# Optimization experiments

Measured on AMD Instinct MI355X. Metric: run time of the kernel, lower is better.

Reference implementation:

```python
import jax, jax.numpy as jnp
import numpy as np

NUM_HEADS = 4
WS = 3


def setup_inputs() -> dict:
    key = jax.random.key(0)
    k1, k2, k3 = jax.random.split(key, 3)
    B, Hs, Ws_, C = 16, 96, 96, 256
    x = jax.random.normal(k1, (B, Hs * Ws_, C), dtype=jnp.float32)
    # torch nn.Linear weights: [out_features, in_features]
    Wqkv = jax.random.normal(k2, (3 * C, C), dtype=jnp.float32) * (1.0 / np.sqrt(C))
    Wproj = jax.random.normal(k3, (C, C), dtype=jnp.float32) * (1.0 / np.sqrt(C))
    return {"x": x, "Wqkv": Wqkv, "Wproj": Wproj, "H": Hs, "W": Ws_}


def reference(x, Wqkv, Wproj, H, W):
    B, N, C = x.shape
    ws = WS
    nh = NUM_HEADS
    hd = C // nh
    scale = hd ** -0.5

    pad_h = (ws - H % ws) % ws
    pad_w = (ws - W % ws) % ws
    xg = x.reshape(B, H, W, C)
    if pad_h > 0 or pad_w > 0:
        xg = jnp.pad(xg, ((0, 0), (0, pad_h), (0, pad_w), (0, 0)))
    H_pad, W_pad = H + pad_h, W + pad_w
    nWh, nWw = H_pad // ws, W_pad // ws
    Bw = B * nWh * nWw

    # window partition: [B, nWh, ws, nWw, ws, C] -> [Bw, ws*ws, C]
    xw = xg.reshape(B, nWh, ws, nWw, ws, C).transpose(0, 1, 3, 2, 4, 5)
    xw = xw.reshape(Bw, ws * ws, C)

    # qkv projection (Linear, no bias): x @ W^T
    qkv = xw @ Wqkv.T                                   # [Bw, 9, 3C]
    qkv = qkv.reshape(Bw, ws * ws, 3, nh, hd).transpose(2, 0, 3, 1, 4)
    q, k, v = qkv[0], qkv[1], qkv[2]                    # [Bw, nh, 9, hd]

    attn = jnp.einsum("bhqd,bhkd->bhqk", q, k) * scale  # [Bw, nh, 9, 9]
    attn = jax.nn.softmax(attn, axis=-1)
    out = jnp.einsum("bhqk,bhkd->bhqd", attn, v)        # [Bw, nh, 9, hd]
    out = out.transpose(0, 2, 1, 3).reshape(Bw, ws * ws, C)
    out = out @ Wproj.T

    # window unpartition
    out = out.reshape(B, nWh, nWw, ws, ws, C).transpose(0, 1, 3, 2, 4, 5)
    out = out.reshape(B, H_pad, W_pad, C)
    if pad_h > 0 or pad_w > 0:
        out = out[:, :H, :W, :]
    return out.reshape(B, H * W, C)
```

## Files before the change

### kernel.cpp

```cpp
#include <hip/hip_runtime.h>
#include <hip/hip_bf16.h>

using f32x4  = __attribute__((ext_vector_type(4))) float;
using bf16x8 = __attribute__((ext_vector_type(8))) short;
using bf16x4 = __attribute__((ext_vector_type(4))) short;
using u32x2  = __attribute__((ext_vector_type(2))) unsigned int;
using u32x4  = __attribute__((ext_vector_type(4))) unsigned int;

__device__ __forceinline__ float bf2f(short s) {
    unsigned u = ((unsigned)(unsigned short)s) << 16;
    return __builtin_bit_cast(float, u);
}
__device__ __forceinline__ unsigned short f2b(float f) {
    unsigned u = __builtin_bit_cast(unsigned, f);
    unsigned r = u + 0x7FFFu + ((u >> 16) & 1u);
    return (unsigned short)(r >> 16);
}
__device__ __forceinline__ void gl_lds16(const void* g, void* l) {
    __builtin_amdgcn_global_load_lds((const __attribute__((address_space(1))) void*)g,
                                     (__attribute__((address_space(3))) void*)l, 16, 0, 0);
}

__global__ void k_wconv(const float* __restrict__ wq, const float* __restrict__ wp,
                        unsigned short* __restrict__ out) {
    int i = blockIdx.x * 256 + threadIdx.x;
    float v = (i < 196608) ? wq[i] : wp[i - 196608];
    out[i] = f2b(v);
}

__global__ __launch_bounds__(256, 3) void k_qkv3(
    const float* __restrict__ x,
    const unsigned short* __restrict__ wqkv,
    unsigned short* __restrict__ qkv)
{
    __shared__ unsigned short As[128 * 64];
    __shared__ unsigned short Bs[128 * 64];
    const int tid = threadIdx.x;
    const int wv = tid >> 6, ln = tid & 63;
    const int lr = ln & 15, lk = ln >> 4;
    const int l8 = ln >> 3, c8 = ln & 7;

    const int b = blockIdx.x;
    const int w = (b & 7) * 864 + (b >> 3);
    const size_t m0 = (size_t)(w / 6) * 128;
    const int n0 = (w % 6) * 128;
    const int mq = (wv >> 1) * 64, nq = (wv & 1) * 64;

    f32x4 acc[4][4];
#pragma unroll
    for (int mi = 0; mi < 4; ++mi)
#pragma unroll
        for (int ni = 0; ni < 4; ++ni) {
            f32x4 z = {0.f, 0.f, 0.f, 0.f};
            acc[mi][ni] = z;
        }

#pragma unroll 1
    for (int ks = 0; ks < 4; ++ks) {
        const int k0 = ks * 64;
        __syncthreads();
#pragma unroll
        for (int i = 0; i < 4; ++i) {
            int r8 = i * 8 + l8;
            int sc = (c8 ^ (r8 & 7)) * 8;
            gl_lds16(wqkv + (size_t)(n0 + wv * 32 + r8) * 256 + k0 + sc,
                     &Bs[(wv * 32 + i * 8) * 64]);
        }
#pragma unroll
        for (int i = 0; i < 4; ++i) {
            int slot = tid + 256 * i;
            int row = slot >> 3, ch = slot & 7;
            const f32x4* p = (const f32x4*)(x + (m0 + row) * 256 + k0 + ch * 8);
            f32x4 f0 = p[0], f1 = p[1];
            bf16x8 v;
#pragma unroll
            for (int j = 0; j < 4; ++j) {
                v[j]     = (short)f2b(f0[j]);
                v[4 + j] = (short)f2b(f1[j]);
            }
            *(bf16x8*)&As[row * 64 + ((ch ^ (row & 7)) * 8)] = v;
        }
        __syncthreads();

#pragma unroll
        for (int kk = 0; kk < 2; ++kk) {
            bf16x8 av[4], bv[4];
#pragma unroll
            for (int i = 0; i < 4; ++i) {
                int ar = mq + i * 16 + lr;
                av[i] = *(const bf16x8*)&As[ar * 64 + (((kk * 4 + lk) ^ (ar & 7)) * 8)];
                int br = nq + i * 16 + lr;
                bv[i] = *(const bf16x8*)&Bs[br * 64 + (((kk * 4 + lk) ^ (br & 7)) * 8)];
            }
#pragma unroll
            for (int mi = 0; mi < 4; ++mi)
#pragma unroll
                for (int ni = 0; ni < 4; ++ni)
                    acc[mi][ni] = __builtin_amdgcn_mfma_f32_16x16x32_bf16(bv[ni], av[mi], acc[mi][ni], 0, 0, 0);
        }
    }

#pragma unroll
    for (int mi = 0; mi < 4; ++mi) {
        const size_t row = m0 + mq + mi * 16 + lr;
#pragma unroll
        for (int ni = 0; ni < 4; ++ni) {
            u32x2 u;
            u[0] = (unsigned)f2b(acc[mi][ni][0]) | ((unsigned)f2b(acc[mi][ni][1]) << 16);
            u[1] = (unsigned)f2b(acc[mi][ni][2]) | ((unsigned)f2b(acc[mi][ni][3]) << 16);
            *(u32x2*)(qkv + row * 768 + n0 + nq + ni * 16 + lk * 4) = u;
        }
    }
}

__global__ __launch_bounds__(256) void k_attn(
    unsigned short* __restrict__ qkv)
{
    constexpr int LQ = 68;
    __shared__ unsigned short Ks[144 * LQ];
    __shared__ unsigned short Vs[144 * LQ];
    const int tid = threadIdx.x;
    const int t3 = blockIdx.x;
    const int hf = blockIdx.y;
    const int h  = blockIdx.z;
    const int bb = t3 >> 5, wh = t3 & 31;

    for (int idx = tid; idx < 1152; idx += 256) {
        int row = idx >> 3, ch = idx & 7;
        int ww = row / 9, t = row - ww * 9;
        int rr = t / 3, cc = t - rr * 3;
        size_t xrow = (size_t)bb * 9216 + (wh * 3 + rr) * 96 + hf * 48 + ww * 3 + cc;
        *(bf16x8*)&Ks[row * LQ + ch * 8] = *(const bf16x8*)(qkv + xrow * 768 + 256 + h * 64 + ch * 8);
        *(bf16x8*)&Vs[row * LQ + ch * 8] = *(const bf16x8*)(qkv + xrow * 768 + 512 + h * 64 + ch * 8);
    }
    __syncthreads();

#pragma unroll 1
    for (int pass = 0; pass < 2; ++pass) {
        int row;
        bool act;
        if (pass == 0) { row = tid >> 1;            act = true; }
        else           { row = 128 + (tid >> 1);    act = tid < 32; }
        if (act) {
            const int hc = tid & 1;
            const int w9 = (row / 9) * 9;
            int t = row - w9;
            int rr = t / 3, cc = t - rr * 3;
            size_t xrow = (size_t)bb * 9216 + (wh * 3 + rr) * 96 + hf * 48 + (w9 / 9) * 3 + cc;
            unsigned short* qp = qkv + xrow * 768 + h * 64 + hc * 32;
            float q[32];
#pragma unroll
            for (int g = 0; g < 4; ++g) {
                bf16x8 v = *(const bf16x8*)(qp + g * 8);
#pragma unroll
                for (int j = 0; j < 8; ++j) q[g * 8 + j] = bf2f(v[j]);
            }
            float s[9];
#pragma unroll
            for (int kk = 0; kk < 9; ++kk) {
                float acc = 0.f;
#pragma unroll
                for (int g = 0; g < 4; ++g) {
                    bf16x8 v = *(const bf16x8*)&Ks[(w9 + kk) * LQ + hc * 32 + g * 8];
#pragma unroll
                    for (int j = 0; j < 8; ++j) acc += q[g * 8 + j] * bf2f(v[j]);
                }
                s[kk] = acc;
            }
#pragma unroll
            for (int kk = 0; kk < 9; ++kk)
                s[kk] = (s[kk] + __shfl_xor(s[kk], 1)) * 0.125f;
            float m = s[0];
#pragma unroll
            for (int kk = 1; kk < 9; ++kk) m = fmaxf(m, s[kk]);
            float sum = 0.f;
#pragma unroll
            for (int kk = 0; kk < 9; ++kk) { s[kk] = __expf(s[kk] - m); sum += s[kk]; }
            float inv = 1.f / sum;
            float o[32];
#pragma unroll
            for (int d = 0; d < 32; ++d) o[d] = 0.f;
#pragma unroll
            for (int kk = 0; kk < 9; ++kk) {
                float pk = s[kk] * inv;
#pragma unroll
                for (int g = 0; g < 4; ++g) {
                    bf16x8 v = *(const bf16x8*)&Vs[(w9 + kk) * LQ + hc * 32 + g * 8];
#pragma unroll
                    for (int j = 0; j < 8; ++j) o[g * 8 + j] += pk * bf2f(v[j]);
                }
            }
#pragma unroll
            for (int grp = 0; grp < 4; ++grp) {
                u32x4 u;
#pragma unroll
                for (int e = 0; e < 4; ++e) {
                    int i0 = grp * 8 + e * 2;
                    u[e] = (unsigned)f2b(o[i0]) | ((unsigned)f2b(o[i0 + 1]) << 16);
                }
                *(u32x4*)(qp + grp * 8) = u;
            }
        }
    }
}

__global__ __launch_bounds__(256) void k_proj(
    const unsigned short* __restrict__ ain,
    const unsigned short* __restrict__ wproj,
    float* __restrict__ out)
{
    __shared__ unsigned short As[128 * 64];
    __shared__ unsigned short Bs[128 * 64];
    const int tid = threadIdx.x;
    const int wv = tid >> 6, ln = tid & 63;
    const int lr = ln & 15, lk = ln >> 4;
    const int l8 = ln >> 3, c8 = ln & 7;

    int b = blockIdx.x;
    int w = (b & 7) * 288 + (b >> 3);
    const size_t m0 = (size_t)(w >> 1) * 128;
    const int n0 = (w & 1) * 128;
    const int mq = (wv >> 1) * 64, nq = (wv & 1) * 64;

    f32x4 acc[4][4];
#pragma unroll
    for (int mi = 0; mi < 4; ++mi)
#pragma unroll
        for (int ni = 0; ni < 4; ++ni) {
            f32x4 z = {0.f, 0.f, 0.f, 0.f};
            acc[mi][ni] = z;
        }

#pragma unroll 1
    for (int ks = 0; ks < 4; ++ks) {
        const int k0 = ks * 64;
        __syncthreads();
#pragma unroll
        for (int i = 0; i < 4; ++i) {
            int r8 = i * 8 + l8;
            int sc = (c8 ^ (r8 & 7)) * 8;
            gl_lds16(ain   + (m0 + wv * 32 + r8) * 768 + k0 + sc,
                     &As[(wv * 32 + i * 8) * 64]);
            gl_lds16(wproj + (size_t)(n0 + wv * 32 + r8) * 256 + k0 + sc,
                     &Bs[(wv * 32 + i * 8) * 64]);
        }
        __syncthreads();

#pragma unroll
        for (int kk = 0; kk < 2; ++kk) {
            bf16x8 av[4], bv[4];
#pragma unroll
            for (int i = 0; i < 4; ++i) {
                int ar = mq + i * 16 + lr;
                av[i] = *(const bf16x8*)&As[ar * 64 + (((kk * 4 + lk) ^ (ar & 7)) * 8)];
                int br = nq + i * 16 + lr;
                bv[i] = *(const bf16x8*)&Bs[br * 64 + (((kk * 4 + lk) ^ (br & 7)) * 8)];
            }
#pragma unroll
            for (int mi = 0; mi < 4; ++mi)
#pragma unroll
                for (int ni = 0; ni < 4; ++ni)
                    acc[mi][ni] = __builtin_amdgcn_mfma_f32_16x16x32_bf16(bv[ni], av[mi], acc[mi][ni], 0, 0, 0);
        }
    }

#pragma unroll
    for (int mi = 0; mi < 4; ++mi) {
        const size_t row = m0 + mq + mi * 16 + lr;
#pragma unroll
        for (int ni = 0; ni < 4; ++ni)
            *(f32x4*)&out[row * 256 + n0 + nq + ni * 16 + lk * 4] = acc[mi][ni];
    }
}


__device__ __forceinline__ int grow_of(int wbase, int row) {
    int wi = row / 9;
    int t  = row - wi * 9;
    int w  = wbase + wi;
    if (w >= 16384) return -1;
    int b = w >> 10, rem = w & 1023;
    int wh = rem >> 5, ww = rem & 31;
    int r = t / 3, c = t - r * 3;
    return b * 9216 + (wh * 3 + r) * 96 + ww * 3 + c;
}

__global__ __launch_bounds__(256) void k_winattn_fb(
    const float* __restrict__ x,
    const unsigned short* __restrict__ wqkv,
    unsigned short* __restrict__ aout)
{
    constexpr int LDA = 264;
    constexpr int LQ  = 68;
    __shared__ unsigned short As[64 * LDA];
    __shared__ unsigned short Qb[3][64 * LQ];
    __shared__ int rowmap[64];

    const int tid = threadIdx.x;
    const int wbase = blockIdx.x * 7;
    const int wv = tid >> 6, ln = tid & 63;
    const int lr = ln & 15, lk = ln >> 4;
    const int mw = wv >> 1, nw = wv & 1;

    if (tid < 64)
        rowmap[tid] = (tid < 63) ? grow_of(wbase, tid) : -1;
    __syncthreads();

    for (int idx = tid; idx < 64 * 32; idx += 256) {
        int row = idx >> 5, g = idx & 31;
        int gr = rowmap[row];
        bf16x8 v;
        if (gr >= 0) {
            const f32x4* p = (const f32x4*)(x + (size_t)gr * 256 + g * 8);
            f32x4 f0 = p[0], f1 = p[1];
#pragma unroll
            for (int j = 0; j < 4; ++j) {
                v[j]     = (short)f2b(f0[j]);
                v[4 + j] = (short)f2b(f1[j]);
            }
        } else {
#pragma unroll
            for (int j = 0; j < 8; ++j) v[j] = 0;
        }
        *(bf16x8*)&As[row * LDA + g * 8] = v;
    }
    __syncthreads();

#pragma unroll 1
    for (int h = 0; h < 4; ++h) {
#pragma unroll 1
        for (int part = 0; part < 3; ++part) {
            const int j0 = part * 256 + h * 64 + nw * 32;
            bf16x8 w[2][8];
#pragma unroll
            for (int ni = 0; ni < 2; ++ni)
#pragma unroll
                for (int kk = 0; kk < 8; ++kk)
                    w[ni][kk] = *(const bf16x8*)(wqkv + (size_t)(j0 + ni * 16 + lr) * 256 + kk * 32 + lk * 8);

            f32x4 acc[2][2];
#pragma unroll
            for (int mi = 0; mi < 2; ++mi)
#pragma unroll
                for (int ni = 0; ni < 2; ++ni) {
                    f32x4 z = {0.f, 0.f, 0.f, 0.f};
                    acc[mi][ni] = z;
                }
#pragma unroll
            for (int kk = 0; kk < 8; ++kk) {
                const int k0 = kk * 32 + lk * 8;
                bf16x8 a0 = *(const bf16x8*)&As[(mw * 32 + lr) * LDA + k0];
                bf16x8 a1 = *(const bf16x8*)&As[(mw * 32 + 16 + lr) * LDA + k0];
                acc[0][0] = __builtin_amdgcn_mfma_f32_16x16x32_bf16(w[0][kk], a0, acc[0][0], 0, 0, 0);
                acc[1][0] = __builtin_amdgcn_mfma_f32_16x16x32_bf16(w[0][kk], a1, acc[1][0], 0, 0, 0);
                acc[0][1] = __builtin_amdgcn_mfma_f32_16x16x32_bf16(w[1][kk], a0, acc[0][1], 0, 0, 0);
                acc[1][1] = __builtin_amdgcn_mfma_f32_16x16x32_bf16(w[1][kk], a1, acc[1][1], 0, 0, 0);
            }
#pragma unroll
            for (int mi = 0; mi < 2; ++mi)
#pragma unroll
                for (int ni = 0; ni < 2; ++ni) {
                    int row = mw * 32 + mi * 16 + lr;
                    int col = nw * 32 + ni * 16 + lk * 4;
                    u32x2 u;
                    u[0] = (unsigned)f2b(acc[mi][ni][0]) | ((unsigned)f2b(acc[mi][ni][1]) << 16);
                    u[1] = (unsigned)f2b(acc[mi][ni][2]) | ((unsigned)f2b(acc[mi][ni][3]) << 16);
                    *(u32x2*)&Qb[part][row * LQ + col] = u;
                }
        }
        __syncthreads();
        {
            const int row = wv * 16 + lr;
            const int c   = lk;
            if (row < 63) {
                const int w9 = (row / 9) * 9;
                float q[16];
#pragma unroll
                for (int g = 0; g < 4; ++g) {
                    bf16x4 v = *(const bf16x4*)&Qb[0][row * LQ + c * 16 + g * 4];
#pragma unroll
                    for (int j = 0; j < 4; ++j) q[g * 4 + j] = bf2f(v[j]);
                }
                float s[9];
#pragma unroll
                for (int kk = 0; kk < 9; ++kk) {
                    float t = 0.f;
#pragma unroll
                    for (int g = 0; g < 4; ++g) {
                        bf16x4 v = *(const bf16x4*)&Qb[1][(w9 + kk) * LQ + c * 16 + g * 4];
#pragma unroll
                        for (int j = 0; j < 4; ++j) t += q[g * 4 + j] * bf2f(v[j]);
                    }
                    s[kk] = t;
                }
#pragma unroll
                for (int kk = 0; kk < 9; ++kk) {
                    float t = s[kk];
                    t += __shfl_xor(t, 16);
                    t += __shfl_xor(t, 32);
                    s[kk] = t * 0.125f;
                }
                float m = s[0];
#pragma unroll
                for (int kk = 1; kk < 9; ++kk) m = fmaxf(m, s[kk]);
                float sum = 0.f;
#pragma unroll
                for (int kk = 0; kk < 9; ++kk) { s[kk] = __expf(s[kk] - m); sum += s[kk]; }
                float inv = 1.f / sum;
                float o[16];
#pragma unroll
                for (int d = 0; d < 16; ++d) o[d] = 0.f;
#pragma unroll
                for (int kk = 0; kk < 9; ++kk) {
                    float pk = s[kk] * inv;
#pragma unroll
                    for (int g = 0; g < 4; ++g) {
                        bf16x4 v = *(const bf16x4*)&Qb[2][(w9 + kk) * LQ + c * 16 + g * 4];
#pragma unroll
                        for (int j = 0; j < 4; ++j) o[g * 4 + j] += pk * bf2f(v[j]);
                    }
                }
                const int gr = rowmap[row];
                if (gr >= 0) {
#pragma unroll
                    for (int half = 0; half < 2; ++half) {
                        u32x4 u;
#pragma unroll
                        for (int e = 0; e < 4; ++e) {
                            int i0 = half * 8 + e * 2;
                            u[e] = (unsigned)f2b(o[i0]) | ((unsigned)f2b(o[i0 + 1]) << 16);
                        }
                        *(u32x4*)(aout + (size_t)gr * 256 + h * 64 + c * 16 + half * 8) = u;
                    }
                }
            }
        }
        __syncthreads();
    }
}

__global__ __launch_bounds__(256) void k_proj_fb(
    const unsigned short* __restrict__ ain,
    const unsigned short* __restrict__ wproj,
    float* __restrict__ out)
{
    const int tid = threadIdx.x;
    const int wv = tid >> 6, ln = tid & 63;
    const int lr = ln & 15, lk = ln >> 4;
    const size_t row0 = (size_t)blockIdx.x * 128;

    bf16x8 af[2][8];
#pragma unroll
    for (int mi = 0; mi < 2; ++mi) {
        const size_t row = row0 + wv * 32 + mi * 16 + lr;
#pragma unroll
        for (int kk = 0; kk < 8; ++kk)
            af[mi][kk] = *(const bf16x8*)(ain + row * 256 + kk * 32 + lk * 8);
    }
#pragma unroll
    for (int nc = 0; nc < 4; ++nc) {
        const int j0 = nc * 64;
        f32x4 acc[2][4];
#pragma unroll
        for (int mi = 0; mi < 2; ++mi)
#pragma unroll
            for (int ni = 0; ni < 4; ++ni) {
                f32x4 z = {0.f, 0.f, 0.f, 0.f};
                acc[mi][ni] = z;
            }
#pragma unroll
        for (int kk = 0; kk < 8; ++kk) {
            bf16x8 w[4];
#pragma unroll
            for (int ni = 0; ni < 4; ++ni)
                w[ni] = *(const bf16x8*)(wproj + (size_t)(j0 + ni * 16 + lr) * 256 + kk * 32 + lk * 8);
#pragma unroll
            for (int ni = 0; ni < 4; ++ni) {
                acc[0][ni] = __builtin_amdgcn_mfma_f32_16x16x32_bf16(w[ni], af[0][kk], acc[0][ni], 0, 0, 0);
                acc[1][ni] = __builtin_amdgcn_mfma_f32_16x16x32_bf16(w[ni], af[1][kk], acc[1][ni], 0, 0, 0);
            }
        }
#pragma unroll
        for (int mi = 0; mi < 2; ++mi) {
            const size_t row = row0 + wv * 32 + mi * 16 + lr;
#pragma unroll
            for (int ni = 0; ni < 4; ++ni)
                *(f32x4*)&out[row * 256 + j0 + ni * 16 + lk * 4] = acc[mi][ni];
        }
    }
}

extern "C" void kernel_launch(void* const* d_in, const int* in_sizes, int n_in,
                              void* d_out, int out_size, void* d_ws, size_t ws_size,
                              hipStream_t stream) {
    const float* x  = (const float*)d_in[0];
    const float* wq = (const float*)d_in[1];
    const float* wp = (const float*)d_in[2];
    unsigned short* wsb     = (unsigned short*)d_ws;
    unsigned short* wqkv_b  = wsb;
    unsigned short* wproj_b = wsb + 196608;
    float* out = (float*)d_out;

    k_wconv<<<1024, 256, 0, stream>>>(wq, wp, wsb);

    const size_t need = 524288ULL + 147456ULL * 768ULL * 2ULL;
    if (ws_size >= need) {
        unsigned short* qkv = wsb + 262144;
        k_qkv3<<<6912, 256, 0, stream>>>(x, wqkv_b, qkv);
        k_attn<<<dim3(512, 2, 4), 256, 0, stream>>>(qkv);
        k_proj<<<2304, 256, 0, stream>>>(qkv, wproj_b, out);
    } else {
        unsigned short* aout = wsb + 262144;
        k_winattn_fb<<<2341, 256, 0, stream>>>(x, wqkv_b, aout);
        k_proj_fb  <<<1152, 256, 0, stream>>>(aout, wproj_b, out);
    }
}
```

Measured before the change: 285.7 us.

## Double-buffer weight tiles and prefetch x into registers in QKV GEMM

Restructures the QKV projection main loop so that the next K-slice of the weight tile is staged into a second LDS buffer and the next x slice is loaded into registers while MFMAs run on the current slice. The goal is to hide global-load latency that the old load-sync-compute loop exposed. The fp32-to-bf16 conversion of x also switches to the HIP intrinsic instead of manual rounding. In exchange, LDS use grows by one extra 16 KB B buffer and each thread holds eight more float4 prefetch registers, which may lower occupancy under launch_bounds(256,3). There are also extra barriers per iteration.

```diff
diff --git a/kernel.cpp b/kernel.cpp
--- a/kernel.cpp
+++ b/kernel.cpp
@@ -16,6 +16,10 @@
     unsigned r = u + 0x7FFFu + ((u >> 16) & 1u);
     return (unsigned short)(r >> 16);
 }
+__device__ __forceinline__ short f2b_hw(float f) {
+    __hip_bfloat16 h = __float2bfloat16(f);
+    return *reinterpret_cast<short*>(&h);
+}
 __device__ __forceinline__ void gl_lds16(const void* g, void* l) {
     __builtin_amdgcn_global_load_lds((const __attribute__((address_space(1))) void*)g,
                                      (__attribute__((address_space(3))) void*)l, 16, 0, 0);
@@ -28,13 +32,13 @@
     out[i] = f2b(v);
 }
 
-__global__ __launch_bounds__(256, 3) void k_qkv3(
+__global__ __launch_bounds__(256, 3) void k_qkv5(
     const float* __restrict__ x,
     const unsigned short* __restrict__ wqkv,
     unsigned short* __restrict__ qkv)
 {
     __shared__ unsigned short As[128 * 64];
-    __shared__ unsigned short Bs[128 * 64];
+    __shared__ unsigned short Bs[2][128 * 64];
     const int tid = threadIdx.x;
     const int wv = tid >> 6, ln = tid & 63;
     const int lr = ln & 15, lk = ln >> 4;
@@ -46,6 +50,43 @@
     const int n0 = (w % 6) * 128;
     const int mq = (wv >> 1) * 64, nq = (wv & 1) * 64;
 
+    f32x4 xv[8];
+
+#define XLOAD(KS)                                                              \
+    {                                                                          \
+        _Pragma("unroll")                                                      \
+        for (int p = 0; p < 4; ++p) {                                          \
+            int row = wv * 32 + p * 8 + l8;                                    \
+            const f32x4* src = (const f32x4*)(x + (m0 + row) * 256 + (KS) * 64 + c8 * 8); \
+            xv[p * 2]     = src[0];                                            \
+            xv[p * 2 + 1] = src[1];                                            \
+        }                                                                      \
+    }
+#define AWRITE()                                                               \
+    {                                                                          \
+        _Pragma("unroll")                                                      \
+        for (int p = 0; p < 4; ++p) {                                          \
+            int row = wv * 32 + p * 8 + l8;                                    \
+            bf16x8 v;                                                          \
+            _Pragma("unroll")                                                  \
+            for (int j = 0; j < 4; ++j) {                                      \
+                v[j]     = f2b_hw(xv[p * 2][j]);                               \
+                v[4 + j] = f2b_hw(xv[p * 2 + 1][j]);                           \
+            }                                                                  \
+            *(bf16x8*)&As[row * 64 + ((c8 ^ (row & 7)) * 8)] = v;              \
+        }                                                                      \
+    }
+#define BSTAGE(KS, BUF)                                                        \
+    {                                                                          \
+        _Pragma("unroll")                                                      \
+        for (int i = 0; i < 4; ++i) {                                          \
+            int r8 = i * 8 + l8;                                               \
+            int sc = (c8 ^ (r8 & 7)) * 8;                                      \
+            gl_lds16(wqkv + (size_t)(n0 + wv * 32 + r8) * 256 + (KS) * 64 + sc,\
+                     &Bs[BUF][(wv * 32 + i * 8) * 64]);                        \
+        }                                                                      \
+    }
+
     f32x4 acc[4][4];
 #pragma unroll
     for (int mi = 0; mi < 4; ++mi)
@@ -55,33 +96,18 @@
             acc[mi][ni] = z;
         }
 
+    BSTAGE(0, 0);
+    XLOAD(0);
+    AWRITE();
+    __syncthreads();
+
+    int buf = 0;
 #pragma unroll 1
     for (int ks = 0; ks < 4; ++ks) {
-        const int k0 = ks * 64;
-        __syncthreads();
-#pragma unroll
-        for (int i = 0; i < 4; ++i) {
-            int r8 = i * 8 + l8;
-            int sc = (c8 ^ (r8 & 7)) * 8;
-            gl_lds16(wqkv + (size_t)(n0 + wv * 32 + r8) * 256 + k0 + sc,
-                     &Bs[(wv * 32 + i * 8) * 64]);
-        }
-#pragma unroll
-        for (int i = 0; i < 4; ++i) {
-            int slot = tid + 256 * i;
-            int row = slot >> 3, ch = slot & 7;
-            const f32x4* p = (const f32x4*)(x + (m0 + row) * 256 + k0 + ch * 8);
-            f32x4 f0 = p[0], f1 = p[1];
-            bf16x8 v;
-#pragma unroll
-            for (int j = 0; j < 4; ++j) {
-                v[j]     = (short)f2b(f0[j]);
-                v[4 + j] = (short)f2b(f1[j]);
-            }
-            *(bf16x8*)&As[row * 64 + ((ch ^ (row & 7)) * 8)] = v;
-        }
-        __syncthreads();
-
+        if (ks < 3) {
+            BSTAGE(ks + 1, buf ^ 1);
+            XLOAD(ks + 1);
+        }
 #pragma unroll
         for (int kk = 0; kk < 2; ++kk) {
             bf16x8 av[4], bv[4];
@@ -90,7 +116,7 @@
                 int ar = mq + i * 16 + lr;
                 av[i] = *(const bf16x8*)&As[ar * 64 + (((kk * 4 + lk) ^ (ar & 7)) * 8)];
                 int br = nq + i * 16 + lr;
-                bv[i] = *(const bf16x8*)&Bs[br * 64 + (((kk * 4 + lk) ^ (br & 7)) * 8)];
+                bv[i] = *(const bf16x8*)&Bs[buf][br * 64 + (((kk * 4 + lk) ^ (br & 7)) * 8)];
             }
 #pragma unroll
             for (int mi = 0; mi < 4; ++mi)
@@ -98,7 +124,15 @@
                 for (int ni = 0; ni < 4; ++ni)
                     acc[mi][ni] = __builtin_amdgcn_mfma_f32_16x16x32_bf16(bv[ni], av[mi], acc[mi][ni], 0, 0, 0);
         }
-    }
+        __syncthreads();
+        if (ks < 3) AWRITE();
+        __syncthreads();
+        buf ^= 1;
+    }
+
+#undef XLOAD
+#undef AWRITE
+#undef BSTAGE
 
 #pragma unroll
     for (int mi = 0; mi < 4; ++mi) {
@@ -506,7 +540,7 @@
     const size_t need = 524288ULL + 147456ULL * 768ULL * 2ULL;
     if (ws_size >= need) {
         unsigned short* qkv = wsb + 262144;
-        k_qkv3<<<6912, 256, 0, stream>>>(x, wqkv_b, qkv);
+        k_qkv5<<<6912, 256, 0, stream>>>(x, wqkv_b, qkv);
         k_attn<<<dim3(512, 2, 4), 256, 0, stream>>>(qkv);
         k_proj<<<2304, 256, 0, stream>>>(qkv, wproj_b, out);
     } else {
```

After: 282.4 us. About the same (-1.2%).
